# Kernel tuning notes

Hardware: AMD Instinct MI355X
Metric: run time of the kernel (lower is better)

The kernel has to match this reference:

```python
import jax, jax.numpy as jnp
import numpy as np

V, T_BLOCK, D, H, L, HS = 32000, 1024, 1024, 16, 6, 64
B, T = 4, 1024
EPS = 1e-5


def setup_inputs() -> dict:
    key = jax.random.key(0)
    ks = jax.random.split(key, 12)
    s = 0.02  # init std, matches _init_weights
    return {
        'input_tokens': jax.random.randint(ks[0], (B, T), 0, V),
        'tok_emb': jax.random.normal(ks[1], (V, D), jnp.float32) * s,
        'pos_emb': jax.random.normal(ks[2], (T_BLOCK, D), jnp.float32) * s,
        'Wq': jax.random.normal(ks[3], (L, H, D, HS), jnp.float32) * s,
        'Wk': jax.random.normal(ks[4], (L, H, D, HS), jnp.float32) * s,
        'Wv': jax.random.normal(ks[5], (L, H, D, HS), jnp.float32) * s,
        'Wo': jax.random.normal(ks[6], (L, D, D), jnp.float32) * s,
        'bo': jnp.zeros((L, D), jnp.float32),
        'ln1_g': jnp.ones((L, D), jnp.float32),
        'ln1_b': jnp.zeros((L, D), jnp.float32),
        'ln2_g': jnp.ones((L, D), jnp.float32),
        'ln2_b': jnp.zeros((L, D), jnp.float32),
        'W1': jax.random.normal(ks[7], (L, D, 4 * D), jnp.float32) * s,
        'b1': jnp.zeros((L, 4 * D), jnp.float32),
        'W2': jax.random.normal(ks[8], (L, 4 * D, D), jnp.float32) * s,
        'b2': jnp.zeros((L, D), jnp.float32),
        'lnf_g': jnp.ones((D,), jnp.float32),
        'lnf_b': jnp.zeros((D,), jnp.float32),
        'W_out': jax.random.normal(ks[9], (D, V), jnp.float32) * s,
        'b_out': jnp.zeros((V,), jnp.float32),
    }


def _layer_norm(x, g, b):
    mu = jnp.mean(x, axis=-1, keepdims=True)
    var = jnp.mean(jnp.square(x - mu), axis=-1, keepdims=True)
    return (x - mu) * jax.lax.rsqrt(var + EPS) * g + b


def _attn(x, Wq, Wk, Wv, Wo, bo, causal_mask):
    # x: [B,T,D]; Wq/Wk/Wv: [H,D,hs] (per-head linears, bias=False)
    q = jnp.einsum('btd,hds->bhts', x, Wq)
    k = jnp.einsum('btd,hds->bhts', x, Wk)
    v = jnp.einsum('btd,hds->bhts', x, Wv)
    scores = jnp.einsum('bhts,bhus->bhtu', q, k) * (HS ** -0.5)
    scores = jnp.where(causal_mask, scores, -jnp.inf)
    w = jax.nn.softmax(scores, axis=-1)  # dropout=0.0 -> identity
    o = jnp.einsum('bhtu,bhus->bhts', w, v)
    # concat heads in order, then projection
    o = o.transpose(0, 2, 1, 3).reshape(x.shape[0], x.shape[1], H * HS)
    return o @ Wo + bo


def reference(input_tokens, tok_emb, pos_emb, Wq, Wk, Wv, Wo, bo,
              ln1_g, ln1_b, ln2_g, ln2_b, W1, b1, W2, b2,
              lnf_g, lnf_b, W_out, b_out):
    Bc, Tc = input_tokens.shape
    x = tok_emb[input_tokens] + pos_emb[:Tc]  # [B,T,D]
    mask = jnp.tril(jnp.ones((Tc, Tc), bool))[None, None]  # [1,1,T,T]
    for l in range(L):
        x = x + _attn(_layer_norm(x, ln1_g[l], ln1_b[l]),
                      Wq[l], Wk[l], Wv[l], Wo[l], bo[l], mask)
        h = _layer_norm(x, ln2_g[l], ln2_b[l])
        x = x + jax.nn.relu(h @ W1[l] + b1[l]) @ W2[l] + b2[l]
    x = _layer_norm(x, lnf_g, lnf_b)
    logits = x @ W_out + b_out  # [B,T,V]
    return logits
```

## Files before the change

### kernel.cpp

```cpp
#include <hip/hip_runtime.h>
#include <hip/hip_bf16.h>

#define HS 64
#define NH 16
#define DMODEL 1024
#define SEQ 1024
#define NB 4
#define NL 6
#define VOCAB 32000
#define EPS_LN 1e-5f

static constexpr int ROWS = NB * SEQ;

typedef float f32x4 __attribute__((ext_vector_type(4)));
typedef short bf16x8 __attribute__((ext_vector_type(8)));
typedef unsigned short u16x8 __attribute__((ext_vector_type(8)));
typedef unsigned short u16x4 __attribute__((ext_vector_type(4)));

__device__ __forceinline__ unsigned short f2b(float f) {
  __hip_bfloat16 h = __float2bfloat16(f);
  return *reinterpret_cast<unsigned short*>(&h);
}
__device__ __forceinline__ void gload_lds16(const void* g, void* l) {
  __builtin_amdgcn_global_load_lds(
      (const __attribute__((address_space(1))) void*)g,
      (__attribute__((address_space(3))) void*)l, 16, 0, 0);
}
#define MFMA16 __builtin_amdgcn_mfma_f32_16x16x32_bf16
#define EXP2F __builtin_amdgcn_exp2f

__global__ __launch_bounds__(256) void embed_kernel(
    const int* __restrict__ tokens, const float* __restrict__ tok_emb,
    const float* __restrict__ pos_emb, float* __restrict__ x) {
  int row = blockIdx.x;
  int t = row & (SEQ - 1);
  int tok = tokens[row];
  int d = threadIdx.x * 4;
  float4 te = *(const float4*)(tok_emb + (size_t)tok * DMODEL + d);
  float4 pe = *(const float4*)(pos_emb + (size_t)t * DMODEL + d);
  te.x += pe.x; te.y += pe.y; te.z += pe.z; te.w += pe.w;
  *(float4*)(x + (size_t)row * DMODEL + d) = te;
}

__global__ __launch_bounds__(256) void ln_kernel(
    const float* __restrict__ in, unsigned short* __restrict__ outp,
    const float* __restrict__ g, const float* __restrict__ b) {
  int row = blockIdx.x;
  int tid = threadIdx.x;
  const float* xr = in + (size_t)row * DMODEL;
  float4 v4 = *(const float4*)(xr + tid * 4);
  float s = v4.x + v4.y + v4.z + v4.w;
  float s2 = v4.x * v4.x + v4.y * v4.y + v4.z * v4.z + v4.w * v4.w;
#pragma unroll
  for (int off = 32; off > 0; off >>= 1) {
    s  += __shfl_down(s, off, 64);
    s2 += __shfl_down(s2, off, 64);
  }
  __shared__ float red[8];
  __shared__ float stats[2];
  int wv = tid >> 6, lane = tid & 63;
  if (lane == 0) { red[wv] = s; red[4 + wv] = s2; }
  __syncthreads();
  if (tid == 0) {
    float ts = red[0] + red[1] + red[2] + red[3];
    float ts2 = red[4] + red[5] + red[6] + red[7];
    float mu = ts * (1.0f / DMODEL);
    float var = ts2 * (1.0f / DMODEL) - mu * mu;
    stats[0] = mu;
    stats[1] = rsqrtf(var + EPS_LN);
  }
  __syncthreads();
  float mu = stats[0], rstd = stats[1];
  float4 g4 = *(const float4*)(g + tid * 4);
  float4 b4 = *(const float4*)(b + tid * 4);
  u16x4 o;
  o[0] = f2b((v4.x - mu) * rstd * g4.x + b4.x);
  o[1] = f2b((v4.y - mu) * rstd * g4.y + b4.y);
  o[2] = f2b((v4.z - mu) * rstd * g4.z + b4.z);
  o[3] = f2b((v4.w - mu) * rstd * g4.w + b4.w);
  *(u16x4*)(outp + (size_t)row * DMODEL + tid * 4) = o;
}

__global__ __launch_bounds__(256) void transconv(
    const float* __restrict__ in, unsigned short* __restrict__ outp, int K, int N) {
  __shared__ float tile[64][33];
  size_t zoff = (size_t)blockIdx.z * K * N;
  in += zoff;
  outp += zoff;
  int n0 = blockIdx.x * 32, k0 = blockIdx.y * 64;
  int tx = threadIdx.x & 31, ty = threadIdx.x >> 5;
#pragma unroll
  for (int i = 0; i < 8; ++i)
    tile[ty + i * 8][tx] = in[(size_t)(k0 + ty + i * 8) * N + n0 + tx];
  __syncthreads();
  int n = threadIdx.x >> 3;
  int kq = (threadIdx.x & 7) * 8;
  u16x8 o8;
#pragma unroll
  for (int j = 0; j < 8; ++j) o8[j] = f2b(tile[kq + j][n]);
  *(u16x8*)(outp + (size_t)(n0 + n) * K + k0 + kq) = o8;
}

__global__ __launch_bounds__(256) void qkv_transconv(
    const float* __restrict__ Wq, const float* __restrict__ Wk,
    const float* __restrict__ Wv, unsigned short* __restrict__ outp) {
  __shared__ float tile[64][33];
  int z = blockIdx.z;
  int l = z / 48;
  int r = z % 48;
  int which = r >> 4, h = r & 15;
  const float* W = (which == 0 ? Wq : which == 1 ? Wk : Wv) +
                   ((size_t)l * NH + h) * DMODEL * HS;
  int s0 = blockIdx.x * 32, d0 = blockIdx.y * 64;
  int tx = threadIdx.x & 31, ty = threadIdx.x >> 5;
#pragma unroll
  for (int i = 0; i < 8; ++i)
    tile[ty + i * 8][tx] = W[(size_t)(d0 + ty + i * 8) * HS + s0 + tx];
  __syncthreads();
  unsigned short* ob = outp + ((size_t)l * 3072 + which * 1024 + h * 64) * DMODEL;
  int n = threadIdx.x >> 3;
  int kq = (threadIdx.x & 7) * 8;
  u16x8 o8;
#pragma unroll
  for (int j = 0; j < 8; ++j) o8[j] = f2b(tile[kq + j][n]);
  *(u16x8*)(ob + (size_t)(s0 + n) * DMODEL + d0 + kq) = o8;
}

#define EPI_LOGITS 0
#define EPI_RES 1
#define EPI_RELU 2
#define EPI_QKV 3

template <int EPI, int BM_>
__global__ __launch_bounds__(512, 2) void mmX(
    const unsigned short* __restrict__ A, const unsigned short* __restrict__ Bt,
    const float* __restrict__ bias, const float* __restrict__ res,
    float* __restrict__ outf, unsigned short* __restrict__ ob0,
    unsigned short* __restrict__ ob1, unsigned short* __restrict__ ob2,
    int M, int N, int K) {
  constexpr int NA = BM_ / 64;
  constexpr int AP = BM_ / 128;
  constexpr int MFRAG = BM_ / 32;
  __shared__ __align__(16) unsigned short LDS[2][(BM_ + 256) * 64];
  const int tid = threadIdx.x;
  const int lane = tid & 63, w = tid >> 6;
  const int wm2 = w >> 2, wn4 = w & 3;
  const int l15 = lane & 15, l4 = lane >> 4;

  const int nM = M / BM_, nN = N >> 8;
  const int nwg = nM * nN;
  int bid = blockIdx.x;
  int wg = (bid & 7) * (nwg >> 3) + (bid >> 3);
  int mb = wg % nM, nb = wg / nM;
  const int m0 = mb * BM_, n0 = nb * 256;

  const int srow = tid >> 3;
  const int scolb = (tid & 7) * 16;
  const int swst = (srow & 7) << 4;
  const char* aS = (const char*)A + ((size_t)(m0 + srow) * K) * 2 + (scolb ^ swst);
  const char* bS = (const char*)Bt + ((size_t)(n0 + srow) * K) * 2 + (scolb ^ swst);
  const size_t rstep = (size_t)64 * K * 2;

  const int kb0 = l4 * 16;
  const int swz = (l15 & 7) << 4;

  const int NT = K >> 6;
  f32x4 acc[MFRAG][4] = {};
  bf16x8 bv[4][2], avA[AP][2], avB[AP][2];

#define STAGEX(tt)                                                          \
  {                                                                         \
    unsigned short* ad = &LDS[(tt) & 1][0] + (size_t)tid * 8;               \
    unsigned short* bd = &LDS[(tt) & 1][BM_ * 64] + (size_t)tid * 8;        \
    size_t ko = (size_t)(tt) * 128;                                         \
    _Pragma("unroll")                                                       \
    for (int j = 0; j < NA; ++j) gload_lds16(aS + ko + j * rstep, ad + j * 4096); \
    _Pragma("unroll")                                                       \
    for (int j = 0; j < 4; ++j) gload_lds16(bS + ko + j * rstep, bd + j * 4096);  \
  }

#define READA(dst, p)                                                       \
  _Pragma("unroll")                                                         \
  for (int mm = 0; mm < AP; ++mm)                                           \
  _Pragma("unroll")                                                         \
    for (int ks = 0; ks < 2; ++ks)                                          \
      dst[mm][ks] = *(const bf16x8*)(ab + (AP * (p) + mm) * 2048 +          \
                                     ((kb0 + 64 * ks) ^ swz));

#define GROUP(src, p)                                                       \
  __builtin_amdgcn_s_setprio(1);                                            \
  _Pragma("unroll")                                                         \
  for (int ks = 0; ks < 2; ++ks)                                            \
  _Pragma("unroll")                                                         \
    for (int mm = 0; mm < AP; ++mm)                                         \
    _Pragma("unroll")                                                       \
      for (int ni = 0; ni < 4; ++ni)                                        \
        acc[AP * (p) + mm][ni] =                                            \
            MFMA16(src[mm][ks], bv[ni][ks], acc[AP * (p) + mm][ni], 0, 0, 0);\
  __builtin_amdgcn_s_setprio(0);

  STAGEX(0)
  STAGEX(1)

  for (int t = 0; t < NT; ++t) {
    if (t < NT - 1) {
      if constexpr (BM_ == 256) asm volatile("s_waitcnt vmcnt(8)" ::: "memory");
      else                      asm volatile("s_waitcnt vmcnt(6)" ::: "memory");
    } else {
      asm volatile("s_waitcnt vmcnt(0)" ::: "memory");
    }
    __builtin_amdgcn_s_barrier();
    __builtin_amdgcn_sched_barrier(0);
    const char* ab = (const char*)&LDS[t & 1][0] +
                     (size_t)(wm2 * (BM_ / 2) + l15) * 128;
    const char* bb = (const char*)&LDS[t & 1][BM_ * 64] +
                     (size_t)(wn4 * 64 + l15) * 128;
#pragma unroll
    for (int ni = 0; ni < 4; ++ni)
#pragma unroll
      for (int ks = 0; ks < 2; ++ks)
        bv[ni][ks] = *(const bf16x8*)(bb + ni * 2048 + ((kb0 + 64 * ks) ^ swz));
    READA(avA, 0)
    READA(avB, 1)
    GROUP(avA, 0)
    READA(avA, 2)
    GROUP(avB, 1)
    READA(avB, 3)
    GROUP(avA, 2)
    asm volatile("s_waitcnt lgkmcnt(0)" ::: "memory");
    __builtin_amdgcn_sched_barrier(0);
    __builtin_amdgcn_s_barrier();
    __builtin_amdgcn_sched_barrier(0);
    if (t + 2 < NT) STAGEX(t + 2)
    GROUP(avB, 3)
  }
#undef STAGEX
#undef READA
#undef GROUP

  int rbase = m0 + wm2 * (BM_ / 2) + (l4 << 2);
  int cbase = n0 + wn4 * 64 + l15;

  if constexpr (EPI == EPI_LOGITS) {
    float* fl = (float*)&LDS[0][0];
#pragma unroll
    for (int half = 0; half < 2; ++half) {
      __syncthreads();
      if (wm2 == half) {
#pragma unroll
        for (int ni = 0; ni < 4; ++ni) {
          float bvv = bias[cbase + ni * 16];
          int cl = wn4 * 64 + l15 + ni * 16;
#pragma unroll
          for (int mi = 0; mi < MFRAG; ++mi) {
            int rl = mi * 16 + (l4 << 2);
#pragma unroll
            for (int r = 0; r < 4; ++r)
              fl[(rl + r) * 256 + cl] = acc[mi][ni][r] + bvv;
          }
        }
      }
      __syncthreads();
#pragma unroll
      for (int j = 0; j < 16; ++j) {
        int idx = j * 512 + tid;
        int rl = idx >> 6;
        int cc = (idx & 63) << 2;
        f32x4 v4 = *(const f32x4*)&fl[rl * 256 + cc];
        float* gp = outf + (size_t)(m0 + half * 128 + rl) * N + n0 + cc;
        __builtin_nontemporal_store(v4, (f32x4*)gp);
      }
    }
  } else {
#pragma unroll
    for (int ni = 0; ni < 4; ++ni) {
      int col = cbase + ni * 16;
      float bvv = 0.f;
      if (EPI != EPI_QKV) bvv = bias[col];
      if (EPI == EPI_QKV) {
        int which = col >> 10;
        int c2 = col & 1023;
        int h = c2 >> 6, s = c2 & 63;
#pragma unroll
        for (int mi = 0; mi < MFRAG; ++mi) {
          f32x4 a4 = acc[mi][ni];
          int row0 = rbase + mi * 16;
          int bb2 = row0 >> 10, t0 = row0 & 1023;
          if (which == 2) {
            u16x4 pk;
            pk[0] = f2b(a4[0]); pk[1] = f2b(a4[1]); pk[2] = f2b(a4[2]); pk[3] = f2b(a4[3]);
            *(u16x4*)(ob2 + ((((size_t)bb2 * NH + h) * HS) + s) * SEQ + t0) = pk;
          } else {
            unsigned short* dst = (which == 0) ? ob0 : ob1;
#pragma unroll
            for (int r = 0; r < 4; ++r)
              dst[((((size_t)bb2 * NH) + h) * SEQ + t0 + r) * HS + s] = f2b(a4[r]);
          }
        }
      } else {
#pragma unroll
        for (int mi = 0; mi < MFRAG; ++mi) {
          f32x4 a4 = acc[mi][ni];
#pragma unroll
          for (int r = 0; r < 4; ++r) {
            int rowg = rbase + mi * 16 + r;
            size_t off = (size_t)rowg * N + col;
            float v = a4[r] + bvv;
            if (EPI == EPI_RES) outf[off] = v + res[off];
            else if (EPI == EPI_RELU) ob0[off] = f2b(fmaxf(v, 0.f));
          }
        }
      }
    }
  }
}

__global__ __launch_bounds__(256) void attn_mfma(
    const unsigned short* __restrict__ q, const unsigned short* __restrict__ k,
    const unsigned short* __restrict__ vt, unsigned short* __restrict__ outp) {
  __shared__ __align__(16) unsigned short S[16384];
  unsigned short* Ks = S;
  unsigned short* Vs = S + 8192;
  int qt = blockIdx.x, bh = blockIdx.y;
  int tid = threadIdx.x;
  int lane = tid & 63, w = tid >> 6;
  int l15 = lane & 15, l4 = lane >> 4;

  const unsigned short* qb = q + (size_t)bh * SEQ * HS;
  const unsigned short* kb = k + (size_t)bh * SEQ * HS;
  const unsigned short* vb = vt + (size_t)bh * HS * SEQ;

  int q_l = w * 16 + l15;
  int q_g = qt * 64 + q_l;
  bf16x8 qf[2];
  qf[0] = *(const bf16x8*)(qb + (size_t)q_g * HS + l4 * 8);
  qf[1] = *(const bf16x8*)(qb + (size_t)q_g * HS + l4 * 8 + 32);

  int i0 = tid, i1 = tid + 256;
  int kOff0 = (i0 >> 7) * 16 * HS + (i0 & 15) * HS + ((i0 >> 4) & 7) * 8;
  int kOff1 = (i1 >> 7) * 16 * HS + (i1 & 15) * HS + ((i1 >> 4) & 7) * 8;
  int vOff0 = ((i0 >> 7) * 16 + (i0 & 15)) * SEQ + ((i0 >> 4) & 7) * 8;
  int vOff1 = ((i1 >> 7) * 16 + (i1 & 15)) * SEQ + ((i1 >> 4) & 7) * 8;

#define ASTAGE(tt)                                                           \
  {                                                                          \
    int bsel = ((tt) & 1) * 4096;                                            \
    const unsigned short* ksrc = kb + (size_t)(tt) * 64 * HS;                \
    gload_lds16(ksrc + kOff0, Ks + bsel + (size_t)i0 * 8);                   \
    gload_lds16(ksrc + kOff1, Ks + bsel + (size_t)i1 * 8);                   \
    gload_lds16(vb + vOff0 + (tt) * 64, Vs + bsel + (size_t)i0 * 8);         \
    gload_lds16(vb + vOff1 + (tt) * 64, Vs + bsel + (size_t)i1 * 8);         \
  }

  f32x4 o[4] = {};
  float mrun = -3e38f, lrun = 0.f;
  int baseLane = 32 * (l4 & 1) + l15;
  bool hi_t = (l4 >> 1) != 0;
  const float CSC = 0.125f * 1.44269504f;
  const float THR = 8.0f / CSC;

  ASTAGE(0)

  for (int kt = 0; kt <= qt; ++kt) {
    asm volatile("s_waitcnt vmcnt(0)" ::: "memory");
    __builtin_amdgcn_s_barrier();
    __builtin_amdgcn_sched_barrier(0);
    if (kt < qt) ASTAGE(kt + 1)
    const unsigned short* Kb = Ks + (kt & 1) * 4096;
    const unsigned short* Vb = Vs + (kt & 1) * 4096;

    f32x4 s[4];
#pragma unroll
    for (int t = 0; t < 4; ++t) {
      bf16x8 kf0 = *(const bf16x8*)(Kb + ((size_t)(t * 8 + l4) * 16 + l15) * 8);
      bf16x8 kf1 = *(const bf16x8*)(Kb + ((size_t)(t * 8 + l4 + 4) * 16 + l15) * 8);
      s[t] = (f32x4){0.f, 0.f, 0.f, 0.f};
      s[t] = MFMA16(kf0, qf[0], s[t], 0, 0, 0);
      s[t] = MFMA16(kf1, qf[1], s[t], 0, 0, 0);
    }

    if (kt == qt) {
      int keybase = kt * 64 + 4 * l4;
#pragma unroll
      for (int t = 0; t < 4; ++t)
#pragma unroll
        for (int r = 0; r < 4; ++r)
          if (keybase + 16 * t + r > q_g) s[t][r] = -3e38f;
    }
    float mx = -3e38f;
#pragma unroll
    for (int t = 0; t < 4; ++t)
#pragma unroll
      for (int r = 0; r < 4; ++r) mx = fmaxf(mx, s[t][r]);
    mx = fmaxf(mx, __shfl_xor(mx, 16, 64));
    mx = fmaxf(mx, __shfl_xor(mx, 32, 64));
    if (!__all(mx - mrun <= THR)) {
      float mnew = fmaxf(mrun, mx);
      float sc = EXP2F((mrun - mnew) * CSC);
      lrun *= sc;
#pragma unroll
      for (int t2 = 0; t2 < 4; ++t2)
#pragma unroll
        for (int r = 0; r < 4; ++r) o[t2][r] *= sc;
      mrun = mnew;
    }
    float mc = mrun * CSC;
    float ps = 0.f;
    float p[4][4];
#pragma unroll
    for (int t = 0; t < 4; ++t)
#pragma unroll
      for (int r = 0; r < 4; ++r) {
        float e = EXP2F(__builtin_fmaf(s[t][r], CSC, -mc));
        p[t][r] = e;
        ps += e;
      }
    ps += __shfl_xor(ps, 16, 64);
    ps += __shfl_xor(ps, 32, 64);
    lrun += ps;

    int pd[4][2];
#pragma unroll
    for (int t = 0; t < 4; ++t)
#pragma unroll
      for (int h = 0; h < 2; ++h)
        pd[t][h] = (int)f2b(p[t][2 * h]) | ((int)f2b(p[t][2 * h + 1]) << 16);

#pragma unroll
    for (int kk = 0; kk < 2; ++kk) {
      int a0 = __shfl(pd[2 * kk][0], baseLane, 64);
      int b0 = __shfl(pd[2 * kk + 1][0], baseLane, 64);
      int a1 = __shfl(pd[2 * kk][1], baseLane, 64);
      int b1 = __shfl(pd[2 * kk + 1][1], baseLane, 64);
      int a2 = __shfl(pd[2 * kk][0], baseLane + 16, 64);
      int b2 = __shfl(pd[2 * kk + 1][0], baseLane + 16, 64);
      int a3 = __shfl(pd[2 * kk][1], baseLane + 16, 64);
      int b3 = __shfl(pd[2 * kk + 1][1], baseLane + 16, 64);
      union { int4 i4; bf16x8 v; } yu;
      yu.i4.x = hi_t ? b0 : a0;
      yu.i4.y = hi_t ? b1 : a1;
      yu.i4.z = hi_t ? b2 : a2;
      yu.i4.w = hi_t ? b3 : a3;
#pragma unroll
      for (int t2 = 0; t2 < 4; ++t2) {
        bf16x8 vf = *(const bf16x8*)(Vb + ((size_t)(t2 * 8 + l4 + 4 * kk) * 16 + l15) * 8);
        o[t2] = MFMA16(vf, yu.v, o[t2], 0, 0, 0);
      }
    }
  }
#undef ASTAGE

  __syncthreads();
  float inv = 1.0f / lrun;
  unsigned short* Ol = S;
#pragma unroll
  for (int t2 = 0; t2 < 4; ++t2) {
    u16x4 p4;
#pragma unroll
    for (int r = 0; r < 4; ++r) p4[r] = f2b(o[t2][r] * inv);
    *(u16x4*)(Ol + (size_t)q_l * 72 + 16 * t2 + 4 * l4) = p4;
  }
  __syncthreads();
  int row = tid >> 2, hs0 = (tid & 3) * 16;
  int bidx = bh >> 4, h = bh & 15;
  size_t gbase = ((size_t)bidx * SEQ + qt * 64 + row) * DMODEL + h * HS + hs0;
  u16x8 r0 = *(const u16x8*)(Ol + (size_t)row * 72 + hs0);
  u16x8 r1 = *(const u16x8*)(Ol + (size_t)row * 72 + hs0 + 8);
  *(u16x8*)(outp + gbase) = r0;
  *(u16x8*)(outp + gbase + 8) = r1;
}

extern "C" void kernel_launch(void* const* d_in, const int* in_sizes, int n_in,
                              void* d_out, int out_size, void* d_ws, size_t ws_size,
                              hipStream_t stream) {
  const int*   tokens  = (const int*)d_in[0];
  const float* tok_emb = (const float*)d_in[1];
  const float* pos_emb = (const float*)d_in[2];
  const float* Wq      = (const float*)d_in[3];
  const float* Wk      = (const float*)d_in[4];
  const float* Wv      = (const float*)d_in[5];
  const float* Wo      = (const float*)d_in[6];
  const float* bo      = (const float*)d_in[7];
  const float* ln1_g   = (const float*)d_in[8];
  const float* ln1_b   = (const float*)d_in[9];
  const float* ln2_g   = (const float*)d_in[10];
  const float* ln2_b   = (const float*)d_in[11];
  const float* W1      = (const float*)d_in[12];
  const float* b1      = (const float*)d_in[13];
  const float* W2      = (const float*)d_in[14];
  const float* b2      = (const float*)d_in[15];
  const float* lnf_g   = (const float*)d_in[16];
  const float* lnf_b   = (const float*)d_in[17];
  const float* W_out   = (const float*)d_in[18];
  const float* b_out   = (const float*)d_in[19];
  float* logits = (float*)d_out;

  char* p = (char*)d_ws;
  float* x = (float*)p;            p += (size_t)ROWS * DMODEL * 4;
  unsigned short* hb = (unsigned short*)p;  p += (size_t)ROWS * DMODEL * 2;
  unsigned short* qb = (unsigned short*)p;  p += (size_t)ROWS * DMODEL * 2;
  unsigned short* kb = (unsigned short*)p;  p += (size_t)ROWS * DMODEL * 2;
  unsigned short* vtb = (unsigned short*)p; p += (size_t)ROWS * DMODEL * 2;
  unsigned short* att = (unsigned short*)p; p += (size_t)ROWS * DMODEL * 2;
  unsigned short* hid = (unsigned short*)p; p += (size_t)ROWS * 4 * DMODEL * 2;
  unsigned short* qkvt = (unsigned short*)p; p += (size_t)NL * 3 * DMODEL * DMODEL * 2;
  unsigned short* wot = (unsigned short*)p;  p += (size_t)NL * DMODEL * DMODEL * 2;
  unsigned short* w1t = (unsigned short*)p;  p += (size_t)NL * 4 * DMODEL * DMODEL * 2;
  unsigned short* w2t = (unsigned short*)p;  p += (size_t)NL * 4 * DMODEL * DMODEL * 2;
  unsigned short* woutt = (unsigned short*)p; p += (size_t)VOCAB * DMODEL * 2;

  transconv<<<dim3(32, 16, NL), 256, 0, stream>>>(Wo, wot, DMODEL, DMODEL);
  transconv<<<dim3(128, 16, NL), 256, 0, stream>>>(W1, w1t, DMODEL, 4 * DMODEL);
  transconv<<<dim3(32, 64, NL), 256, 0, stream>>>(W2, w2t, 4 * DMODEL, DMODEL);
  transconv<<<dim3(1000, 16, 1), 256, 0, stream>>>(W_out, woutt, DMODEL, VOCAB);
  qkv_transconv<<<dim3(2, 16, NL * 48), 256, 0, stream>>>(Wq, Wk, Wv, qkvt);

  embed_kernel<<<ROWS, 256, 0, stream>>>(tokens, tok_emb, pos_emb, x);

  for (int l = 0; l < NL; ++l) {
    ln_kernel<<<ROWS, 256, 0, stream>>>(x, hb, ln1_g + l * DMODEL, ln1_b + l * DMODEL);
    mmX<EPI_QKV, 256><<<192, 512, 0, stream>>>(
        hb, qkvt + (size_t)l * 3 * DMODEL * DMODEL, nullptr, nullptr,
        nullptr, qb, kb, vtb, ROWS, 3 * DMODEL, DMODEL);
    attn_mfma<<<dim3(SEQ / 64, NB * NH), 256, 0, stream>>>(qb, kb, vtb, att);
    mmX<EPI_RES, 128><<<128, 512, 0, stream>>>(
        att, wot + (size_t)l * DMODEL * DMODEL, bo + l * DMODEL, x,
        x, nullptr, nullptr, nullptr, ROWS, DMODEL, DMODEL);
    ln_kernel<<<ROWS, 256, 0, stream>>>(x, hb, ln2_g + l * DMODEL, ln2_b + l * DMODEL);
    mmX<EPI_RELU, 256><<<256, 512, 0, stream>>>(
        hb, w1t + (size_t)l * 4 * DMODEL * DMODEL, b1 + (size_t)l * 4 * DMODEL, nullptr,
        nullptr, hid, nullptr, nullptr, ROWS, 4 * DMODEL, DMODEL);
    mmX<EPI_RES, 128><<<128, 512, 0, stream>>>(
        hid, w2t + (size_t)l * 4 * DMODEL * DMODEL, b2 + l * DMODEL, x,
        x, nullptr, nullptr, nullptr, ROWS, DMODEL, 4 * DMODEL);
  }

  ln_kernel<<<ROWS, 256, 0, stream>>>(x, hb, lnf_g, lnf_b);
  mmX<EPI_LOGITS, 256><<<2000, 512, 0, stream>>>(
      hb, woutt, b_out, nullptr, logits, nullptr, nullptr, nullptr,
      ROWS, VOCAB, DMODEL);
}
```

Before: 1.828 ms.

## Add 128x128 swizzled GEMM for residual projections, widen attention key tiles

Adds a new 256-thread, 128x128-tile GEMM kernel (mmP) with XOR-swizzled LDS, double-buffered direct-to-LDS loads, and XCD-aware block remapping, and uses it for the Wo and W2 residual projections. These previously ran on only 128 workgroups, so the new kernel raises parallelism to 256 tiles. The attention kernel now processes 128 keys per iteration instead of 64, with larger LDS buffers, to halve loop and sync overhead. The QKV GEMM switches to a 128 tile variant with 384 blocks. Larger attention tiles add register and LDS pressure, and the last tile wastes more masked work on the causal diagonal.

```diff
diff --git a/kernel.cpp b/kernel.cpp
--- a/kernel.cpp
+++ b/kernel.cpp
@@ -315,12 +315,125 @@
   }
 }
 
+template <int EPI>
+__global__ __launch_bounds__(256, 2) void mmP(
+    const unsigned short* __restrict__ A, const unsigned short* __restrict__ Bt,
+    const float* __restrict__ bias, const float* __restrict__ res,
+    float* __restrict__ outf, unsigned short* __restrict__ ob0,
+    int M, int N, int K) {
+  __shared__ __align__(16) unsigned short LDS[2][16384];
+  const int tid = threadIdx.x;
+  const int lane = tid & 63, w = tid >> 6;
+  const int wm2 = w >> 1, wn2 = w & 1;
+  const int l15 = lane & 15, l4 = lane >> 4;
+
+  const int nM = M >> 7, nN = N >> 7;
+  const int nwg = nM * nN;
+  int bid = blockIdx.x;
+  int wg = (bid & 7) * (nwg >> 3) + (bid >> 3);
+  int mb = wg % nM, nb = wg / nM;
+  const int m0 = mb * 128, n0 = nb * 128;
+
+  const int srow = tid >> 3;
+  const int scolb = (tid & 7) * 16;
+  const int swst = (srow & 7) << 4;
+  const char* aS = (const char*)A + ((size_t)(m0 + srow) * K) * 2 + (scolb ^ swst);
+  const char* bS = (const char*)Bt + ((size_t)(n0 + srow) * K) * 2 + (scolb ^ swst);
+  const size_t rstep = (size_t)32 * K * 2;
+
+  const int kb0 = l4 * 16;
+  const int swz = (l15 & 7) << 4;
+
+  const int NT = K >> 6;
+  f32x4 acc[4][4] = {};
+  bf16x8 bv[4][2];
+
+#define STAGEX(tt)                                                          \
+  {                                                                         \
+    unsigned short* ad = &LDS[(tt) & 1][0] + (size_t)tid * 8;               \
+    unsigned short* bd = &LDS[(tt) & 1][8192] + (size_t)tid * 8;            \
+    size_t ko = (size_t)(tt) * 128;                                         \
+    _Pragma("unroll")                                                       \
+    for (int j = 0; j < 4; ++j) gload_lds16(aS + ko + j * rstep, ad + j * 2048); \
+    _Pragma("unroll")                                                       \
+    for (int j = 0; j < 4; ++j) gload_lds16(bS + ko + j * rstep, bd + j * 2048); \
+  }
+
+#define RDA(dst, mi)                                                        \
+  dst##k0 = *(const bf16x8*)(ab + (mi) * 2048 + (kb0 ^ swz));               \
+  dst##k1 = *(const bf16x8*)(ab + (mi) * 2048 + ((kb0 + 64) ^ swz));
+
+#define GROUP(src, mi)                                                      \
+  __builtin_amdgcn_s_setprio(1);                                            \
+  _Pragma("unroll")                                                         \
+  for (int ni = 0; ni < 4; ++ni)                                            \
+    acc[mi][ni] = MFMA16(src##k0, bv[ni][0], acc[mi][ni], 0, 0, 0);         \
+  _Pragma("unroll")                                                         \
+  for (int ni = 0; ni < 4; ++ni)                                            \
+    acc[mi][ni] = MFMA16(src##k1, bv[ni][1], acc[mi][ni], 0, 0, 0);         \
+  __builtin_amdgcn_s_setprio(0);
+
+  STAGEX(0)
+  STAGEX(1)
+
+  for (int t = 0; t < NT; ++t) {
+    if (t < NT - 1) asm volatile("s_waitcnt vmcnt(8)" ::: "memory");
+    else            asm volatile("s_waitcnt vmcnt(0)" ::: "memory");
+    __builtin_amdgcn_s_barrier();
+    __builtin_amdgcn_sched_barrier(0);
+    const char* ab = (const char*)&LDS[t & 1][0] + (size_t)(wm2 * 64 + l15) * 128;
+    const char* bb = (const char*)&LDS[t & 1][8192] + (size_t)(wn2 * 64 + l15) * 128;
+    bf16x8 aEk0, aEk1, aOk0, aOk1;
+#pragma unroll
+    for (int ni = 0; ni < 4; ++ni) {
+      bv[ni][0] = *(const bf16x8*)(bb + ni * 2048 + (kb0 ^ swz));
+      bv[ni][1] = *(const bf16x8*)(bb + ni * 2048 + ((kb0 + 64) ^ swz));
+    }
+    RDA(aE, 0)
+    GROUP(aE, 0)
+    RDA(aO, 1)
+    GROUP(aO, 1)
+    RDA(aE, 2)
+    GROUP(aE, 2)
+    RDA(aO, 3)
+    asm volatile("s_waitcnt lgkmcnt(0)" ::: "memory");
+    __builtin_amdgcn_sched_barrier(0);
+    __builtin_amdgcn_s_barrier();
+    __builtin_amdgcn_sched_barrier(0);
+    if (t + 2 < NT) STAGEX(t + 2)
+    GROUP(aO, 3)
+  }
+#undef STAGEX
+#undef RDA
+#undef GROUP
+
+  int rbase = m0 + wm2 * 64 + (l4 << 2);
+  int cbase = n0 + wn2 * 64 + l15;
+#pragma unroll
+  for (int ni = 0; ni < 4; ++ni) {
+    int col = cbase + ni * 16;
+    float bvv = bias[col];
+#pragma unroll
+    for (int mi = 0; mi < 4; ++mi) {
+      f32x4 a4 = acc[mi][ni];
+#pragma unroll
+      for (int r = 0; r < 4; ++r) {
+        int rowg = rbase + mi * 16 + r;
+        size_t off = (size_t)rowg * N + col;
+        float v = a4[r] + bvv;
+        if (EPI == EPI_RES) outf[off] = v + res[off];
+        else if (EPI == EPI_RELU) ob0[off] = f2b(fmaxf(v, 0.f));
+      }
+    }
+  }
+}
+
 __global__ __launch_bounds__(256) void attn_mfma(
     const unsigned short* __restrict__ q, const unsigned short* __restrict__ k,
     const unsigned short* __restrict__ vt, unsigned short* __restrict__ outp) {
-  __shared__ __align__(16) unsigned short S[16384];
+  __shared__ __align__(16) unsigned short S[32768];
   unsigned short* Ks = S;
-  unsigned short* Vs = S + 8192;
+  unsigned short* Vs = S + 16384;
   int qt = blockIdx.x, bh = blockIdx.y;
   int tid = threadIdx.x;
   int lane = tid & 63, w = tid >> 6;
@@ -336,20 +449,25 @@
   qf[0] = *(const bf16x8*)(qb + (size_t)q_g * HS + l4 * 8);
   qf[1] = *(const bf16x8*)(qb + (size_t)q_g * HS + l4 * 8 + 32);
 
-  int i0 = tid, i1 = tid + 256;
-  int kOff0 = (i0 >> 7) * 16 * HS + (i0 & 15) * HS + ((i0 >> 4) & 7) * 8;
-  int kOff1 = (i1 >> 7) * 16 * HS + (i1 & 15) * HS + ((i1 >> 4) & 7) * 8;
-  int vOff0 = ((i0 >> 7) * 16 + (i0 & 15)) * SEQ + ((i0 >> 4) & 7) * 8;
-  int vOff1 = ((i1 >> 7) * 16 + (i1 & 15)) * SEQ + ((i1 >> 4) & 7) * 8;
+  int kOff[4], vOff[4];
+#pragma unroll
+  for (int j = 0; j < 4; ++j) {
+    int idx = tid + j * 256;
+    kOff[j] = (idx >> 7) * 16 * HS + (idx & 15) * HS + ((idx >> 4) & 7) * 8;
+    vOff[j] = ((idx >> 8) * 16 + (idx & 15)) * SEQ + ((idx >> 4) & 15) * 8;
+  }
 
 #define ASTAGE(tt)                                                           \
   {                                                                          \
-    int bsel = ((tt) & 1) * 4096;                                            \
-    const unsigned short* ksrc = kb + (size_t)(tt) * 64 * HS;                \
-    gload_lds16(ksrc + kOff0, Ks + bsel + (size_t)i0 * 8);                   \
-    gload_lds16(ksrc + kOff1, Ks + bsel + (size_t)i1 * 8);                   \
-    gload_lds16(vb + vOff0 + (tt) * 64, Vs + bsel + (size_t)i0 * 8);         \
-    gload_lds16(vb + vOff1 + (tt) * 64, Vs + bsel + (size_t)i1 * 8);         \
+    int bsel = ((tt) & 1) * 8192;                                            \
+    const unsigned short* ksrc = kb + (size_t)(tt) * 128 * HS;               \
+    const unsigned short* vsrc = vb + (tt) * 128;                            \
+    _Pragma("unroll")                                                        \
+    for (int j = 0; j < 4; ++j)                                              \
+      gload_lds16(ksrc + kOff[j], Ks + bsel + (size_t)(tid + j * 256) * 8);  \
+    _Pragma("unroll")                                                        \
+    for (int j = 0; j < 4; ++j)                                              \
+      gload_lds16(vsrc + vOff[j], Vs + bsel + (size_t)(tid + j * 256) * 8);  \
   }
 
   f32x4 o[4] = {};
@@ -359,19 +477,20 @@
   const float CSC = 0.125f * 1.44269504f;
   const float THR = 8.0f / CSC;
 
+  int nt2 = (qt + 2) >> 1;
   ASTAGE(0)
 
-  for (int kt = 0; kt <= qt; ++kt) {
+  for (int kt = 0; kt < nt2; ++kt) {
     asm volatile("s_waitcnt vmcnt(0)" ::: "memory");
     __builtin_amdgcn_s_barrier();
     __builtin_amdgcn_sched_barrier(0);
-    if (kt < qt) ASTAGE(kt + 1)
-    const unsigned short* Kb = Ks + (kt & 1) * 4096;
-    const unsigned short* Vb = Vs + (kt & 1) * 4096;
-
-    f32x4 s[4];
-#pragma unroll
-    for (int t = 0; t < 4; ++t) {
+    if (kt + 1 < nt2) ASTAGE(kt + 1)
+    const unsigned short* Kb = Ks + (kt & 1) * 8192;
+    const unsigned short* Vb = Vs + (kt & 1) * 8192;
+
+    f32x4 s[8];
+#pragma unroll
+    for (int t = 0; t < 8; ++t) {
       bf16x8 kf0 = *(const bf16x8*)(Kb + ((size_t)(t * 8 + l4) * 16 + l15) * 8);
       bf16x8 kf1 = *(const bf16x8*)(Kb + ((size_t)(t * 8 + l4 + 4) * 16 + l15) * 8);
       s[t] = (f32x4){0.f, 0.f, 0.f, 0.f};
@@ -379,17 +498,17 @@
       s[t] = MFMA16(kf1, qf[1], s[t], 0, 0, 0);
     }
 
-    if (kt == qt) {
-      int keybase = kt * 64 + 4 * l4;
-#pragma unroll
-      for (int t = 0; t < 4; ++t)
+    if (kt == nt2 - 1) {
+      int keybase = kt * 128 + 4 * l4;
+#pragma unroll
+      for (int t = 0; t < 8; ++t)
 #pragma unroll
         for (int r = 0; r < 4; ++r)
           if (keybase + 16 * t + r > q_g) s[t][r] = -3e38f;
     }
     float mx = -3e38f;
 #pragma unroll
-    for (int t = 0; t < 4; ++t)
+    for (int t = 0; t < 8; ++t)
 #pragma unroll
       for (int r = 0; r < 4; ++r) mx = fmaxf(mx, s[t][r]);
     mx = fmaxf(mx, __shfl_xor(mx, 16, 64));
@@ -406,28 +525,27 @@
     }
     float mc = mrun * CSC;
     float ps = 0.f;
-    float p[4][4];
-#pragma unroll
-    for (int t = 0; t < 4; ++t)
+#pragma unroll
+    for (int t = 0; t < 8; ++t)
 #pragma unroll
       for (int r = 0; r < 4; ++r) {
         float e = EXP2F(__builtin_fmaf(s[t][r], CSC, -mc));
-        p[t][r] = e;
+        s[t][r] = e;
         ps += e;
       }
     ps += __shfl_xor(ps, 16, 64);
     ps += __shfl_xor(ps, 32, 64);
     lrun += ps;
 
-    int pd[4][2];
-#pragma unroll
-    for (int t = 0; t < 4; ++t)
+    int pd[8][2];
+#pragma unroll
+    for (int t = 0; t < 8; ++t)
 #pragma unroll
       for (int h = 0; h < 2; ++h)
-        pd[t][h] = (int)f2b(p[t][2 * h]) | ((int)f2b(p[t][2 * h + 1]) << 16);
-
-#pragma unroll
-    for (int kk = 0; kk < 2; ++kk) {
+        pd[t][h] = (int)f2b(s[t][2 * h]) | ((int)f2b(s[t][2 * h + 1]) << 16);
+
+#pragma unroll
+    for (int kk = 0; kk < 4; ++kk) {
       int a0 = __shfl(pd[2 * kk][0], baseLane, 64);
       int b0 = __shfl(pd[2 * kk + 1][0], baseLane, 64);
       int a1 = __shfl(pd[2 * kk][1], baseLane, 64);
@@ -443,7 +561,7 @@
       yu.i4.w = hi_t ? b3 : a3;
 #pragma unroll
       for (int t2 = 0; t2 < 4; ++t2) {
-        bf16x8 vf = *(const bf16x8*)(Vb + ((size_t)(t2 * 8 + l4 + 4 * kk) * 16 + l15) * 8);
+        bf16x8 vf = *(const bf16x8*)(Vb + ((size_t)(t2 * 16 + kk * 4 + l4) * 16 + l15) * 8);
         o[t2] = MFMA16(vf, yu.v, o[t2], 0, 0, 0);
       }
     }
@@ -519,20 +637,20 @@
 
   for (int l = 0; l < NL; ++l) {
     ln_kernel<<<ROWS, 256, 0, stream>>>(x, hb, ln1_g + l * DMODEL, ln1_b + l * DMODEL);
-    mmX<EPI_QKV, 256><<<192, 512, 0, stream>>>(
+    mmX<EPI_QKV, 128><<<384, 512, 0, stream>>>(
         hb, qkvt + (size_t)l * 3 * DMODEL * DMODEL, nullptr, nullptr,
         nullptr, qb, kb, vtb, ROWS, 3 * DMODEL, DMODEL);
     attn_mfma<<<dim3(SEQ / 64, NB * NH), 256, 0, stream>>>(qb, kb, vtb, att);
-    mmX<EPI_RES, 128><<<128, 512, 0, stream>>>(
+    mmP<EPI_RES><<<256, 256, 0, stream>>>(
         att, wot + (size_t)l * DMODEL * DMODEL, bo + l * DMODEL, x,
-        x, nullptr, nullptr, nullptr, ROWS, DMODEL, DMODEL);
+        x, nullptr, ROWS, DMODEL, DMODEL);
     ln_kernel<<<ROWS, 256, 0, stream>>>(x, hb, ln2_g + l * DMODEL, ln2_b + l * DMODEL);
     mmX<EPI_RELU, 256><<<256, 512, 0, stream>>>(
         hb, w1t + (size_t)l * 4 * DMODEL * DMODEL, b1 + (size_t)l * 4 * DMODEL, nullptr,
         nullptr, hid, nullptr, nullptr, ROWS, 4 * DMODEL, DMODEL);
-    mmX<EPI_RES, 128><<<128, 512, 0, stream>>>(
+    mmP<EPI_RES><<<256, 256, 0, stream>>>(
         hid, w2t + (size_t)l * 4 * DMODEL * DMODEL, b2 + l * DMODEL, x,
-        x, nullptr, nullptr, nullptr, ROWS, DMODEL, 4 * DMODEL);
+        x, nullptr, ROWS, DMODEL, 4 * DMODEL);
   }
 
   ln_kernel<<<ROWS, 256, 0, stream>>>(x, hb, lnf_g, lnf_b);
```

Result: faster. 1.776 ms (-2.9%).
